# Optimization experiments

Measured on AMD Instinct MI355X. Metric: run time of the kernel, lower is better.

The kernel has to match this reference:

```python
import jax, jax.numpy as jnp
import numpy as np

B, T, N, D, TXT, TE, H = 8, 8192, 256, 512, 768, 2048, 8
DH = D // H


def _ln(x, g, b):
    m = jnp.mean(x, axis=-1, keepdims=True)
    v = jnp.mean(jnp.square(x - m), axis=-1, keepdims=True)
    return (x - m) * jax.lax.rsqrt(v + 1e-5) * g + b


def setup_inputs() -> dict:
    key = jax.random.key(0)
    ks = jax.random.split(key, 10)
    s = 0.02  # init scale for weights (zero_module init replaced by small random for a non-trivial baseline)
    return {
        "x": jax.random.normal(ks[0], (B, T, D), jnp.float32),
        "xf": jax.random.normal(ks[1], (B, N, TXT), jnp.float32),
        "emb": jax.random.normal(ks[2], (B, TE), jnp.float32),
        "ln_x_g": jnp.ones((D,), jnp.float32),
        "ln_x_b": jnp.zeros((D,), jnp.float32),
        "ln_t_g": jnp.ones((TXT,), jnp.float32),
        "ln_t_b": jnp.zeros((TXT,), jnp.float32),
        "Wq": jax.random.normal(ks[3], (D, D), jnp.float32) * s,
        "bq": jnp.zeros((D,), jnp.float32),
        "Wk": jax.random.normal(ks[4], (TXT, D), jnp.float32) * s,
        "bk": jnp.zeros((D,), jnp.float32),
        "Wv": jax.random.normal(ks[5], (TXT, D), jnp.float32) * s,
        "bv": jnp.zeros((D,), jnp.float32),
        "emb_W": jax.random.normal(ks[6], (TE, 2 * D), jnp.float32) * s,
        "emb_b": jnp.zeros((2 * D,), jnp.float32),
        "ln_o_g": jnp.ones((D,), jnp.float32),
        "ln_o_b": jnp.zeros((D,), jnp.float32),
        "out_W": jax.random.normal(ks[7], (D, D), jnp.float32) * s,
        "out_b": jnp.zeros((D,), jnp.float32),
    }


def reference(x, xf, emb, ln_x_g, ln_x_b, ln_t_g, ln_t_b, Wq, bq, Wk, bk, Wv, bv,
              emb_W, emb_b, ln_o_g, ln_o_b, out_W, out_b):
    xt = _ln(xf, ln_t_g, ln_t_b)                                  # [B,N,TXT]
    q = jax.nn.softmax((_ln(x, ln_x_g, ln_x_b) @ Wq + bq).reshape(B, T, H, DH), axis=-1)
    k = jax.nn.softmax((xt @ Wk + bk).reshape(B, N, H, DH), axis=-1)
    v = (xt @ Wv + bv).reshape(B, N, H, DH)
    attn = jnp.einsum('bnhd,bnhl->bhdl', k, v)                    # [B,H,DH,DH] kv aggregation
    out = jnp.einsum('bthd,bhdl->bthl', q, attn).reshape(B, T, D)  # [B,T,D]
    # StylizationBlock
    eo = (jax.nn.silu(emb) @ emb_W + emb_b)[:, None, :]           # [B,1,2D]
    scale, shift = jnp.split(eo, 2, axis=2)
    h = _ln(out, ln_o_g, ln_o_b) * (1 + scale) + shift
    h = jax.nn.silu(h) @ out_W + out_b
    return x + h
```

## Files before the change

kernel.cpp:

```cpp
#include <hip/hip_runtime.h>
#include <hip/hip_bf16.h>
#include <math.h>

#define Bc 8
#define Tc 8192
#define NTOK 256
#define Dc 512
#define TXT 768
#define TEc 2048
#define Hc 8
#define DHc 64
#define MROWS (Bc * Tc)

typedef __attribute__((ext_vector_type(8))) short bf16x8v;
typedef __attribute__((ext_vector_type(8))) unsigned short u16x8;
typedef __attribute__((ext_vector_type(4))) unsigned short u16x4;
typedef __attribute__((ext_vector_type(4))) float f32x4;

#define MFMA16(a, b, c) __builtin_amdgcn_mfma_f32_16x16x32_bf16(a, b, c, 0, 0, 0)

__device__ __forceinline__ unsigned short f2bf(float f) {
    __hip_bfloat16 h = __float2bfloat16(f);
    return __builtin_bit_cast(unsigned short, h);
}
__device__ __forceinline__ float bf2f(unsigned short u) {
    unsigned int x = ((unsigned int)u) << 16;
    return __builtin_bit_cast(float, x);
}

typedef __attribute__((address_space(3))) unsigned int lds_u32_t;
typedef __attribute__((address_space(1))) const unsigned int gbl_u32_t;
__device__ __forceinline__ void gload16(const unsigned short* g, short* l) {
    __builtin_amdgcn_global_load_lds((gbl_u32_t*)g, (lds_u32_t*)l, 16, 0, 0);
}

__device__ __forceinline__ float warp32_reduce_sum(float v) {
    v += __shfl_xor(v, 16); v += __shfl_xor(v, 8); v += __shfl_xor(v, 4);
    v += __shfl_xor(v, 2);  v += __shfl_xor(v, 1);
    return v;
}

__device__ __forceinline__ void transpose_tile(const float* __restrict__ src,
                                               unsigned short* __restrict__ dst,
                                               int N, int rs, int k0, int n0) {
    __shared__ float tile[64][65];
    int tx = threadIdx.x & 63, tq = threadIdx.x >> 6;
#pragma unroll
    for (int i = 0; i < 16; ++i) {
        int kk = tq + i * 4;
        tile[kk][tx] = src[(size_t)(k0 + kk) * N + n0 + tx];
    }
    __syncthreads();
#pragma unroll
    for (int i = 0; i < 16; ++i) {
        int nn = tq + i * 4;
        dst[(size_t)(n0 + nn) * rs + k0 + tx] = f2bf(tile[tx][nn]);
    }
}

__global__ void __launch_bounds__(256) prep_kernel(
    const float* __restrict__ Wq, const float* __restrict__ oW,
    const float* __restrict__ Wk, const float* __restrict__ Wv,
    const float* __restrict__ xf, const float* __restrict__ ln_t_g,
    const float* __restrict__ ln_t_b,
    unsigned short* __restrict__ Wqt, unsigned short* __restrict__ oWt,
    unsigned short* __restrict__ Wkvt, unsigned short* __restrict__ xt) {
    int bid = blockIdx.x;
    if (bid < 64) {
        transpose_tile(Wq, Wqt, Dc, Dc, (bid >> 3) * 64, (bid & 7) * 64);
        return;
    }
    if (bid < 128) {
        int i = bid - 64;
        transpose_tile(oW, oWt, Dc, Dc, (i >> 3) * 64, (i & 7) * 64);
        return;
    }
    if (bid < 224) {
        int i = bid - 128;
        transpose_tile(Wk, Wkvt, Dc, TXT, (i >> 3) * 64, (i & 7) * 64);
        return;
    }
    if (bid < 320) {
        int i = bid - 224;
        transpose_tile(Wv, Wkvt + (size_t)512 * TXT, Dc, TXT, (i >> 3) * 64, (i & 7) * 64);
        return;
    }
    int w = threadIdx.x >> 6, l = threadIdx.x & 63;
    int row = (bid - 320) * 4 + w;
    const float* src = xf + (size_t)row * TXT;
    float4 a0 = *(const float4*)&src[l * 12];
    float4 a1 = *(const float4*)&src[l * 12 + 4];
    float4 a2 = *(const float4*)&src[l * 12 + 8];
    float vals[12] = {a0.x, a0.y, a0.z, a0.w, a1.x, a1.y, a1.z, a1.w,
                      a2.x, a2.y, a2.z, a2.w};
    float s = 0.f, ss = 0.f;
#pragma unroll
    for (int j = 0; j < 12; ++j) { s += vals[j]; ss += vals[j] * vals[j]; }
#pragma unroll
    for (int m = 1; m <= 32; m <<= 1) { s += __shfl_xor(s, m); ss += __shfl_xor(ss, m); }
    float mean = s * (1.f / TXT), var = ss * (1.f / TXT) - mean * mean;
    float rs = rsqrtf(var + 1e-5f);
    unsigned short o[12];
#pragma unroll
    for (int j = 0; j < 12; ++j) {
        int c = l * 12 + j;
        o[j] = f2bf((vals[j] - mean) * rs * ln_t_g[c] + ln_t_b[c]);
    }
    unsigned short* dp = xt + (size_t)row * TXT + l * 12;
    *(u16x4*)&dp[0] = *(u16x4*)&o[0];
    *(u16x4*)&dp[4] = *(u16x4*)&o[4];
    *(u16x4*)&dp[8] = *(u16x4*)&o[8];
}

__global__ void __launch_bounds__(256) ln_x_kernel(const float* __restrict__ x,
                                                   const float* __restrict__ g,
                                                   const float* __restrict__ bt,
                                                   unsigned short* __restrict__ A1) {
    int w = threadIdx.x >> 6, l = threadIdx.x & 63;
    int row = blockIdx.x * 4 + w;
    const float* src = x + (size_t)row * Dc;
    float4 a0 = *(const float4*)&src[l * 8];
    float4 a1 = *(const float4*)&src[l * 8 + 4];
    float vals[8] = {a0.x, a0.y, a0.z, a0.w, a1.x, a1.y, a1.z, a1.w};
    float s = 0.f, ss = 0.f;
#pragma unroll
    for (int j = 0; j < 8; ++j) { s += vals[j]; ss += vals[j] * vals[j]; }
#pragma unroll
    for (int m = 1; m <= 32; m <<= 1) { s += __shfl_xor(s, m); ss += __shfl_xor(ss, m); }
    float mean = s * (1.f / Dc), var = ss * (1.f / Dc) - mean * mean;
    float rs = rsqrtf(var + 1e-5f);
    u16x8 o;
#pragma unroll
    for (int j = 0; j < 8; ++j) {
        int c = l * 8 + j;
        o[j] = f2bf((vals[j] - mean) * rs * g[c] + bt[c]);
    }
    *(u16x8*)&A1[(size_t)row * Dc + l * 8] = o;
}

__global__ void __launch_bounds__(256) kvgemm_kernel(
    const unsigned short* __restrict__ xt, const unsigned short* __restrict__ Wkvt,
    const float* __restrict__ bk, const float* __restrict__ bv,
    unsigned short* __restrict__ kbuf, unsigned short* __restrict__ vbuf) {
    __shared__ short lds_s[16384];
    short* Alds = lds_s;
    short* Blds = lds_s + 8192;

    const int tid = threadIdx.x, l = tid & 63, w = tid >> 6;
    const int lr = l & 15, lg = l >> 4;
    int mt = blockIdx.x >> 3, nt = blockIdx.x & 7;
    int row0 = mt * 128, col0 = nt * 128;
    int wrow = (w >> 1) * 64, wcol = (w & 1) * 64;

    f32x4 acc[4][4] = {};
    const int cbase = w * 64 + l;

    for (int ks = 0; ks < 12; ++ks) {
#pragma unroll
        for (int i = 0; i < 4; ++i) {
            int c = i * 256 + cbase;
            int r = c >> 3, kc = c & 7;
            int koff = ks * 64 + ((kc ^ (r & 7)) << 3);
            gload16(xt + (size_t)(row0 + r) * TXT + koff, &Alds[((i * 4 + w) * 64) * 8]);
            gload16(Wkvt + (size_t)(col0 + r) * TXT + koff, &Blds[((i * 4 + w) * 64) * 8]);
        }
        __syncthreads();
#pragma unroll
        for (int kk = 0; kk < 2; ++kk) {
            int kcw = kk * 4 + lg;
            bf16x8v af[4], bfr[4];
#pragma unroll
            for (int i = 0; i < 4; ++i) {
                int r = wrow + i * 16 + lr;
                af[i] = *(bf16x8v*)&Alds[(r * 8 + (kcw ^ (r & 7))) * 8];
            }
#pragma unroll
            for (int j = 0; j < 4; ++j) {
                int n = wcol + j * 16 + lr;
                bfr[j] = *(bf16x8v*)&Blds[(n * 8 + (kcw ^ (n & 7))) * 8];
            }
#pragma unroll
            for (int i = 0; i < 4; ++i)
#pragma unroll
                for (int j = 0; j < 4; ++j)
                    acc[i][j] = MFMA16(af[i], bfr[j], acc[i][j]);
        }
        __syncthreads();
    }

    const bool kHalf = (col0 + wcol) < 512;
    int cj[4];
    float bias[4];
#pragma unroll
    for (int j = 0; j < 4; ++j) {
        cj[j] = col0 + wcol + j * 16 + lr;
        bias[j] = kHalf ? bk[cj[j]] : bv[cj[j] - 512];
    }
#pragma unroll
    for (int i = 0; i < 4; ++i)
#pragma unroll
        for (int reg = 0; reg < 4; ++reg) {
            float v0 = acc[i][0][reg] + bias[0], v1 = acc[i][1][reg] + bias[1];
            float v2 = acc[i][2][reg] + bias[2], v3 = acc[i][3][reg] + bias[3];
            if (kHalf) {
                float m = fmaxf(fmaxf(v0, v1), fmaxf(v2, v3));
                m = fmaxf(m, __shfl_xor(m, 1)); m = fmaxf(m, __shfl_xor(m, 2));
                m = fmaxf(m, __shfl_xor(m, 4)); m = fmaxf(m, __shfl_xor(m, 8));
                float e0 = __expf(v0 - m), e1 = __expf(v1 - m);
                float e2 = __expf(v2 - m), e3 = __expf(v3 - m);
                float ssum = e0 + e1 + e2 + e3;
                ssum += __shfl_xor(ssum, 1); ssum += __shfl_xor(ssum, 2);
                ssum += __shfl_xor(ssum, 4); ssum += __shfl_xor(ssum, 8);
                float inv = 1.f / ssum;
                v0 = e0 * inv; v1 = e1 * inv; v2 = e2 * inv; v3 = e3 * inv;
            }
            int r = row0 + wrow + i * 16 + 4 * lg + reg;
            float vv[4] = {v0, v1, v2, v3};
#pragma unroll
            for (int j = 0; j < 4; ++j) {
                if (kHalf) kbuf[(size_t)r * Dc + cj[j]] = f2bf(vv[j]);
                else       vbuf[(size_t)r * Dc + cj[j] - 512] = f2bf(vv[j]);
            }
        }
}

__global__ void __launch_bounds__(512) attn_kernel(const unsigned short* __restrict__ kbuf,
                                                   const unsigned short* __restrict__ vbuf,
                                                   unsigned short* __restrict__ attn_t) {
    __shared__ unsigned short ksh[128][DHc], vsh[128][DHc];
    const int tid = threadIdx.x;
    const int b = blockIdx.x >> 3, h = blockIdx.x & 7;
    const int d = tid >> 3, lb = (tid & 7) * 8;
    const int tok = tid >> 2, c0 = (tid & 3) * 16;
    float acc[8] = {0.f};
    for (int st = 0; st < 2; ++st) {
        __syncthreads();
        size_t o = (size_t)(b * NTOK + st * 128 + tok) * Dc + h * DHc + c0;
        *(u16x8*)&ksh[tok][c0]     = *(const u16x8*)&kbuf[o];
        *(u16x8*)&ksh[tok][c0 + 8] = *(const u16x8*)&kbuf[o + 8];
        *(u16x8*)&vsh[tok][c0]     = *(const u16x8*)&vbuf[o];
        *(u16x8*)&vsh[tok][c0 + 8] = *(const u16x8*)&vbuf[o + 8];
        __syncthreads();
        for (int n = 0; n < 128; ++n) {
            float kd = bf2f(ksh[n][d]);
            u16x4 va = *(const u16x4*)&vsh[n][lb];
            u16x4 vb = *(const u16x4*)&vsh[n][lb + 4];
#pragma unroll
            for (int e = 0; e < 4; ++e) acc[e] += kd * bf2f(va[e]);
#pragma unroll
            for (int e = 0; e < 4; ++e) acc[4 + e] += kd * bf2f(vb[e]);
        }
    }
    size_t base = (size_t)(b * 8 + h) * DHc * DHc;
#pragma unroll
    for (int e = 0; e < 8; ++e)
        attn_t[base + (size_t)(lb + e) * DHc + d] = f2bf(acc[e]);
}

__global__ void __launch_bounds__(256) emb_kernel(const float* __restrict__ emb,
                                                  const float* __restrict__ emb_W,
                                                  const float* __restrict__ emb_b,
                                                  float* __restrict__ eo) {
    __shared__ float s[4][TEc];
    __shared__ float red[4][64][4];
    const int tid = threadIdx.x;
    const int chunk = blockIdx.x >> 1, bh = blockIdx.x & 1;
#pragma unroll
    for (int j = 0; j < 8; ++j) {
        int idx = tid + 256 * j;
        int bi = idx >> 9, kk4 = (idx & 511) * 4;
#pragma unroll
        for (int e = 0; e < 4; ++e) {
            float v = emb[(bh * 4 + bi) * TEc + kk4 + e];
            s[bi][kk4 + e] = v / (1.f + __expf(-v));
        }
    }
    __syncthreads();
    int c = tid & 63, q = tid >> 6;
    int col = chunk * 64 + c;
    float acc[4] = {0.f, 0.f, 0.f, 0.f};
    for (int kk = q * 512; kk < q * 512 + 512; ++kk) {
        float wv = emb_W[(size_t)kk * (2 * Dc) + col];
#pragma unroll
        for (int bi = 0; bi < 4; ++bi) acc[bi] += s[bi][kk] * wv;
    }
#pragma unroll
    for (int bi = 0; bi < 4; ++bi) red[q][c][bi] = acc[bi];
    __syncthreads();
    if (q == 0) {
        float bb = emb_b[col];
#pragma unroll
        for (int bi = 0; bi < 4; ++bi)
            eo[(bh * 4 + bi) * (2 * Dc) + col] =
                red[0][c][bi] + red[1][c][bi] + red[2][c][bi] + red[3][c][bi] + bb;
    }
}

__global__ void __launch_bounds__(512, 4) gemm1_kernel(
    const unsigned short* __restrict__ A1, const unsigned short* __restrict__ Wt,
    const float* __restrict__ bq, const unsigned short* __restrict__ attn_t,
    unsigned short* __restrict__ out1) {
    __shared__ short lds_s[24576];
    short* Alds = lds_s;
    short* Blds = lds_s + 16384;

    const int tid = threadIdx.x, l = tid & 63, w = tid >> 6;
    const int lr = l & 15, lg = l >> 4;
    int raw = blockIdx.x;
    int swz = (raw & 7) * 128 + (raw >> 3);
    int mt = swz >> 2, nt = swz & 3;
    int row0 = mt * 256, col0 = nt * 128;
    int b = row0 >> 13;
    int wrow = (w >> 1) * 64, wcol = (w & 1) * 64;

    f32x4 acc[4][4] = {};

    for (int ks = 0; ks < 8; ++ks) {
#pragma unroll
        for (int i = 0; i < 4; ++i) {
            int c = i * 512 + tid;
            int r = c >> 3, kc = c & 7;
            int koff = ks * 64 + ((kc ^ (r & 7)) << 3);
            gload16(A1 + (size_t)(row0 + r) * Dc + koff, &Alds[(i * 8 + w) * 512]);
        }
#pragma unroll
        for (int i = 0; i < 2; ++i) {
            int c = i * 512 + tid;
            int r = c >> 3, kc = c & 7;
            int koff = ks * 64 + ((kc ^ (r & 7)) << 3);
            gload16(Wt + (size_t)(col0 + r) * Dc + koff, &Blds[(i * 8 + w) * 512]);
        }
        __syncthreads();
#pragma unroll
        for (int kk = 0; kk < 2; ++kk) {
            int kcw = kk * 4 + lg;
            bf16x8v af[4], bfr[4];
#pragma unroll
            for (int i = 0; i < 4; ++i) {
                int r = wrow + i * 16 + lr;
                af[i] = *(bf16x8v*)&Alds[(r * 8 + (kcw ^ (r & 7))) * 8];
            }
#pragma unroll
            for (int j = 0; j < 4; ++j) {
                int n = wcol + j * 16 + lr;
                bfr[j] = *(bf16x8v*)&Blds[(n * 8 + (kcw ^ (n & 7))) * 8];
            }
#pragma unroll
            for (int i = 0; i < 4; ++i)
#pragma unroll
                for (int j = 0; j < 4; ++j)
                    acc[i][j] = MFMA16(af[i], bfr[j], acc[i][j]);
        }
        __syncthreads();
    }

    float bqv[4];
#pragma unroll
    for (int j = 0; j < 4; ++j) bqv[j] = bq[col0 + wcol + j * 16 + lr];

    int hw = nt * 2 + (w & 1);
    const unsigned short* at = attn_t + (size_t)(b * 8 + hw) * DHc * DHc;
    short* Qw = lds_s + w * 1024;

#pragma unroll
    for (int i = 0; i < 4; ++i) {
#pragma unroll
        for (int reg = 0; reg < 4; ++reg) {
            float v0 = acc[i][0][reg] + bqv[0], v1 = acc[i][1][reg] + bqv[1];
            float v2 = acc[i][2][reg] + bqv[2], v3 = acc[i][3][reg] + bqv[3];
            float m = fmaxf(fmaxf(v0, v1), fmaxf(v2, v3));
            m = fmaxf(m, __shfl_xor(m, 1)); m = fmaxf(m, __shfl_xor(m, 2));
            m = fmaxf(m, __shfl_xor(m, 4)); m = fmaxf(m, __shfl_xor(m, 8));
            float e0 = __expf(v0 - m), e1 = __expf(v1 - m);
            float e2 = __expf(v2 - m), e3 = __expf(v3 - m);
            float ssum = e0 + e1 + e2 + e3;
            ssum += __shfl_xor(ssum, 1); ssum += __shfl_xor(ssum, 2);
            ssum += __shfl_xor(ssum, 4); ssum += __shfl_xor(ssum, 8);
            float inv = 1.f / ssum;
            acc[i][0][reg] = e0 * inv; acc[i][1][reg] = e1 * inv;
            acc[i][2][reg] = e2 * inv; acc[i][3][reg] = e3 * inv;
        }
#pragma unroll
        for (int j = 0; j < 4; ++j)
#pragma unroll
            for (int reg = 0; reg < 4; ++reg) {
                int rl = 4 * lg + reg;
                int c = j * 16 + lr;
                Qw[(rl * 8 + ((c >> 3) ^ (rl & 7))) * 8 + (c & 7)] =
                    (short)f2bf(acc[i][j][reg]);
            }
        f32x4 acc2[4] = {};
#pragma unroll
        for (int kk = 0; kk < 2; ++kk) {
            int kc = kk * 4 + lg;
            bf16x8v a = *(bf16x8v*)&Qw[(lr * 8 + (kc ^ (lr & 7))) * 8];
            bf16x8v bf2[4];
#pragma unroll
            for (int j = 0; j < 4; ++j)
                bf2[j] = *(const bf16x8v*)&at[(j * 16 + lr) * DHc + kk * 32 + lg * 8];
#pragma unroll
            for (int j = 0; j < 4; ++j)
                acc2[j] = MFMA16(a, bf2[j], acc2[j]);
        }
#pragma unroll
        for (int j = 0; j < 4; ++j)
#pragma unroll
            for (int reg = 0; reg < 4; ++reg) {
                int r = row0 + wrow + i * 16 + 4 * lg + reg;
                int c = col0 + wcol + j * 16 + lr;
                out1[(size_t)r * Dc + c] = f2bf(acc2[j][reg]);
            }
    }
}

__global__ void __launch_bounds__(256) mid_kernel(const unsigned short* __restrict__ out1,
                                                  const float* __restrict__ eo,
                                                  const float* __restrict__ g,
                                                  const float* __restrict__ bt,
                                                  unsigned short* __restrict__ A2) {
    int w = threadIdx.x >> 6, l = threadIdx.x & 63;
    int row = blockIdx.x * 4 + w;
    int b = row >> 13;
    u16x8 iv = *(const u16x8*)&out1[(size_t)row * Dc + l * 8];
    float vals[8];
    float s = 0.f, ss = 0.f;
#pragma unroll
    for (int j = 0; j < 8; ++j) {
        vals[j] = bf2f(iv[j]);
        s += vals[j]; ss += vals[j] * vals[j];
    }
#pragma unroll
    for (int m = 1; m <= 32; m <<= 1) { s += __shfl_xor(s, m); ss += __shfl_xor(ss, m); }
    float mean = s * (1.f / Dc), var = ss * (1.f / Dc) - mean * mean;
    float rs = rsqrtf(var + 1e-5f);
    const float* scl = eo + (size_t)b * (2 * Dc);
    const float* shf = scl + Dc;
    u16x8 o;
#pragma unroll
    for (int j = 0; j < 8; ++j) {
        int c = l * 8 + j;
        float t = (vals[j] - mean) * rs * g[c] + bt[c];
        t = t * (1.f + scl[c]) + shf[c];
        t = t / (1.f + __expf(-t));
        o[j] = f2bf(t);
    }
    *(u16x8*)&A2[(size_t)row * Dc + l * 8] = o;
}

__global__ void __launch_bounds__(512, 4) gemm2_kernel(
    const unsigned short* __restrict__ A2, const unsigned short* __restrict__ Wt,
    const float* __restrict__ ob, const float* __restrict__ x,
    float* __restrict__ out) {
    __shared__ short lds_s[24576];
    short* Alds = lds_s;
    short* Blds = lds_s + 16384;

    const int tid = threadIdx.x, l = tid & 63, w = tid >> 6;
    const int lr = l & 15, lg = l >> 4;
    int raw = blockIdx.x;
    int swz = (raw & 7) * 128 + (raw >> 3);
    int mt = swz >> 2, nt = swz & 3;
    int row0 = mt * 256, col0 = nt * 128;
    int wrow = (w >> 1) * 64, wcol = (w & 1) * 64;

    f32x4 acc[4][4] = {};

    for (int ks = 0; ks < 8; ++ks) {
#pragma unroll
        for (int i = 0; i < 4; ++i) {
            int c = i * 512 + tid;
            int r = c >> 3, kc = c & 7;
            int koff = ks * 64 + ((kc ^ (r & 7)) << 3);
            gload16(A2 + (size_t)(row0 + r) * Dc + koff, &Alds[(i * 8 + w) * 512]);
        }
#pragma unroll
        for (int i = 0; i < 2; ++i) {
            int c = i * 512 + tid;
            int r = c >> 3, kc = c & 7;
            int koff = ks * 64 + ((kc ^ (r & 7)) << 3);
            gload16(Wt + (size_t)(col0 + r) * Dc + koff, &Blds[(i * 8 + w) * 512]);
        }
        __syncthreads();
#pragma unroll
        for (int kk = 0; kk < 2; ++kk) {
            int kcw = kk * 4 + lg;
            bf16x8v af[4], bfr[4];
#pragma unroll
            for (int i = 0; i < 4; ++i) {
                int r = wrow + i * 16 + lr;
                af[i] = *(bf16x8v*)&Alds[(r * 8 + (kcw ^ (r & 7))) * 8];
            }
#pragma unroll
            for (int j = 0; j < 4; ++j) {
                int n = wcol + j * 16 + lr;
                bfr[j] = *(bf16x8v*)&Blds[(n * 8 + (kcw ^ (n & 7))) * 8];
            }
#pragma unroll
            for (int i = 0; i < 4; ++i)
#pragma unroll
                for (int j = 0; j < 4; ++j)
                    acc[i][j] = MFMA16(af[i], bfr[j], acc[i][j]);
        }
        __syncthreads();
    }

    float obv[4];
#pragma unroll
    for (int j = 0; j < 4; ++j) obv[j] = ob[col0 + wcol + j * 16 + lr];
#pragma unroll
    for (int i = 0; i < 4; ++i)
#pragma unroll
        for (int j = 0; j < 4; ++j)
#pragma unroll
            for (int reg = 0; reg < 4; ++reg) {
                int r = row0 + wrow + i * 16 + 4 * lg + reg;
                int c = col0 + wcol + j * 16 + lr;
                size_t o = (size_t)r * Dc + c;
                out[o] = acc[i][j][reg] + obv[j] + x[o];
            }
}

extern "C" void kernel_launch(void* const* d_in, const int* in_sizes, int n_in,
                              void* d_out, int out_size, void* d_ws, size_t ws_size,
                              hipStream_t stream) {
    const float* x      = (const float*)d_in[0];
    const float* xf     = (const float*)d_in[1];
    const float* emb    = (const float*)d_in[2];
    const float* ln_x_g = (const float*)d_in[3];
    const float* ln_x_b = (const float*)d_in[4];
    const float* ln_t_g = (const float*)d_in[5];
    const float* ln_t_b = (const float*)d_in[6];
    const float* Wq     = (const float*)d_in[7];
    const float* bq     = (const float*)d_in[8];
    const float* Wk     = (const float*)d_in[9];
    const float* bk     = (const float*)d_in[10];
    const float* Wv     = (const float*)d_in[11];
    const float* bv     = (const float*)d_in[12];
    const float* emb_W  = (const float*)d_in[13];
    const float* emb_b  = (const float*)d_in[14];
    const float* ln_o_g = (const float*)d_in[15];
    const float* ln_o_b = (const float*)d_in[16];
    const float* out_W  = (const float*)d_in[17];
    const float* out_b  = (const float*)d_in[18];
    float* out = (float*)d_out;

    unsigned short* xt   = (unsigned short*)d_ws;
    unsigned short* kbuf = xt + (size_t)2048 * TXT;
    unsigned short* vbuf = kbuf + (size_t)2048 * 512;
    unsigned short* Wkvt = vbuf + (size_t)2048 * 512;
    unsigned short* Wqt  = Wkvt + (size_t)1024 * TXT;
    unsigned short* oWt  = Wqt + (size_t)512 * 512;
    unsigned short* attn_t = oWt + (size_t)512 * 512;
    float* eo = (float*)(attn_t + (size_t)64 * 64 * 64);
    unsigned short* out1 = (unsigned short*)(eo + 8 * 1024);
    unsigned short* A1   = out1 + (size_t)MROWS * Dc;
    unsigned short* A2   = A1;

    hipLaunchKernelGGL(prep_kernel, dim3(832), dim3(256), 0, stream,
                       Wq, out_W, Wk, Wv, xf, ln_t_g, ln_t_b, Wqt, oWt, Wkvt, xt);
    hipLaunchKernelGGL(ln_x_kernel, dim3(MROWS / 4), dim3(256), 0, stream,
                       x, ln_x_g, ln_x_b, A1);
    hipLaunchKernelGGL(kvgemm_kernel, dim3(16 * 8), dim3(256), 0, stream,
                       xt, Wkvt, bk, bv, kbuf, vbuf);
    hipLaunchKernelGGL(attn_kernel, dim3(Bc * Hc), dim3(512), 0, stream,
                       kbuf, vbuf, attn_t);
    hipLaunchKernelGGL(emb_kernel, dim3(32), dim3(256), 0, stream, emb, emb_W, emb_b, eo);
    hipLaunchKernelGGL(gemm1_kernel, dim3(MROWS / 256 * 4), dim3(512), 0, stream,
                       A1, Wqt, bq, attn_t, out1);
    hipLaunchKernelGGL(mid_kernel, dim3(MROWS / 4), dim3(256), 0, stream,
                       out1, eo, ln_o_g, ln_o_b, A2);
    hipLaunchKernelGGL(gemm2_kernel, dim3(MROWS / 256 * 4), dim3(512), 0, stream,
                       A2, oWt, out_b, x, out);
}
```

Baseline: 298.5 us.

## Double-buffer LDS tiles and shrink GEMM blocks to 128x128 with 256 threads

Both large GEMM kernels now prefetch the next K-slice into a second LDS buffer with async global-to-LDS loads while MFMAs run on the current slice. This replaces the old load-then-sync-then-compute loop. Block tiles drop from 256x128 with 512 threads to 128x128 with 256 threads, launch bounds change, and the grid doubles. The aim is to hide global load latency behind compute and improve scheduling, at the cost of more LDS per block and more redundant weight-tile loads.

```diff
diff --git a/kernel.cpp b/kernel.cpp
--- a/kernel.cpp
+++ b/kernel.cpp
@@ -32,12 +32,6 @@
 typedef __attribute__((address_space(1))) const unsigned int gbl_u32_t;
 __device__ __forceinline__ void gload16(const unsigned short* g, short* l) {
     __builtin_amdgcn_global_load_lds((gbl_u32_t*)g, (lds_u32_t*)l, 16, 0, 0);
-}
-
-__device__ __forceinline__ float warp32_reduce_sum(float v) {
-    v += __shfl_xor(v, 16); v += __shfl_xor(v, 8); v += __shfl_xor(v, 4);
-    v += __shfl_xor(v, 2);  v += __shfl_xor(v, 1);
-    return v;
 }
 
 __device__ __forceinline__ void transpose_tile(const float* __restrict__ src,
@@ -296,41 +290,56 @@
     }
 }
 
-__global__ void __launch_bounds__(512, 4) gemm1_kernel(
+
+__global__ void __launch_bounds__(256, 2) gemm1_kernel(
     const unsigned short* __restrict__ A1, const unsigned short* __restrict__ Wt,
     const float* __restrict__ bq, const unsigned short* __restrict__ attn_t,
     unsigned short* __restrict__ out1) {
-    __shared__ short lds_s[24576];
-    short* Alds = lds_s;
-    short* Blds = lds_s + 16384;
+    __shared__ short lds_s[32768];
 
     const int tid = threadIdx.x, l = tid & 63, w = tid >> 6;
     const int lr = l & 15, lg = l >> 4;
     int raw = blockIdx.x;
-    int swz = (raw & 7) * 128 + (raw >> 3);
+    int swz = (raw & 7) * 256 + (raw >> 3);
     int mt = swz >> 2, nt = swz & 3;
-    int row0 = mt * 256, col0 = nt * 128;
+    int row0 = mt * 128, col0 = nt * 128;
     int b = row0 >> 13;
     int wrow = (w >> 1) * 64, wcol = (w & 1) * 64;
+    const int cbase = w * 64 + l;
 
     f32x4 acc[4][4] = {};
 
+    {
+        short* Ad = lds_s;
+        short* Bd = lds_s + 8192;
+#pragma unroll
+        for (int i = 0; i < 4; ++i) {
+            int c = i * 256 + cbase;
+            int r = c >> 3, kc = c & 7;
+            int koff = ((kc ^ (r & 7)) << 3);
+            gload16(A1 + (size_t)(row0 + r) * Dc + koff, &Ad[((i * 4 + w) * 64) * 8]);
+            gload16(Wt + (size_t)(col0 + r) * Dc + koff, &Bd[((i * 4 + w) * 64) * 8]);
+        }
+    }
+    __syncthreads();
+
     for (int ks = 0; ks < 8; ++ks) {
-#pragma unroll
-        for (int i = 0; i < 4; ++i) {
-            int c = i * 512 + tid;
-            int r = c >> 3, kc = c & 7;
-            int koff = ks * 64 + ((kc ^ (r & 7)) << 3);
-            gload16(A1 + (size_t)(row0 + r) * Dc + koff, &Alds[(i * 8 + w) * 512]);
-        }
-#pragma unroll
-        for (int i = 0; i < 2; ++i) {
-            int c = i * 512 + tid;
-            int r = c >> 3, kc = c & 7;
-            int koff = ks * 64 + ((kc ^ (r & 7)) << 3);
-            gload16(Wt + (size_t)(col0 + r) * Dc + koff, &Blds[(i * 8 + w) * 512]);
-        }
-        __syncthreads();
+        int cur = ks & 1;
+        if (ks < 7) {
+            short* Ad = lds_s + (cur ^ 1) * 16384;
+            short* Bd = Ad + 8192;
+            int koff0 = (ks + 1) * 64;
+#pragma unroll
+            for (int i = 0; i < 4; ++i) {
+                int c = i * 256 + cbase;
+                int r = c >> 3, kc = c & 7;
+                int koff = koff0 + ((kc ^ (r & 7)) << 3);
+                gload16(A1 + (size_t)(row0 + r) * Dc + koff, &Ad[((i * 4 + w) * 64) * 8]);
+                gload16(Wt + (size_t)(col0 + r) * Dc + koff, &Bd[((i * 4 + w) * 64) * 8]);
+            }
+        }
+        short* Alds = lds_s + cur * 16384;
+        short* Blds = Alds + 8192;
 #pragma unroll
         for (int kk = 0; kk < 2; ++kk) {
             int kcw = kk * 4 + lg;
@@ -358,7 +367,7 @@
 #pragma unroll
     for (int j = 0; j < 4; ++j) bqv[j] = bq[col0 + wcol + j * 16 + lr];
 
-    int hw = nt * 2 + (w & 1);
+    int hw = nt * 2 + (wcol >> 6);
     const unsigned short* at = attn_t + (size_t)(b * 8 + hw) * DHc * DHc;
     short* Qw = lds_s + w * 1024;
 
@@ -447,40 +456,54 @@
     *(u16x8*)&A2[(size_t)row * Dc + l * 8] = o;
 }
 
-__global__ void __launch_bounds__(512, 4) gemm2_kernel(
+__global__ void __launch_bounds__(256, 2) gemm2_kernel(
     const unsigned short* __restrict__ A2, const unsigned short* __restrict__ Wt,
     const float* __restrict__ ob, const float* __restrict__ x,
     float* __restrict__ out) {
-    __shared__ short lds_s[24576];
-    short* Alds = lds_s;
-    short* Blds = lds_s + 16384;
+    __shared__ short lds_s[32768];
 
     const int tid = threadIdx.x, l = tid & 63, w = tid >> 6;
     const int lr = l & 15, lg = l >> 4;
     int raw = blockIdx.x;
-    int swz = (raw & 7) * 128 + (raw >> 3);
+    int swz = (raw & 7) * 256 + (raw >> 3);
     int mt = swz >> 2, nt = swz & 3;
-    int row0 = mt * 256, col0 = nt * 128;
+    int row0 = mt * 128, col0 = nt * 128;
     int wrow = (w >> 1) * 64, wcol = (w & 1) * 64;
+    const int cbase = w * 64 + l;
 
     f32x4 acc[4][4] = {};
 
+    {
+        short* Ad = lds_s;
+        short* Bd = lds_s + 8192;
+#pragma unroll
+        for (int i = 0; i < 4; ++i) {
+            int c = i * 256 + cbase;
+            int r = c >> 3, kc = c & 7;
+            int koff = ((kc ^ (r & 7)) << 3);
+            gload16(A2 + (size_t)(row0 + r) * Dc + koff, &Ad[((i * 4 + w) * 64) * 8]);
+            gload16(Wt + (size_t)(col0 + r) * Dc + koff, &Bd[((i * 4 + w) * 64) * 8]);
+        }
+    }
+    __syncthreads();
+
     for (int ks = 0; ks < 8; ++ks) {
-#pragma unroll
-        for (int i = 0; i < 4; ++i) {
-            int c = i * 512 + tid;
-            int r = c >> 3, kc = c & 7;
-            int koff = ks * 64 + ((kc ^ (r & 7)) << 3);
-            gload16(A2 + (size_t)(row0 + r) * Dc + koff, &Alds[(i * 8 + w) * 512]);
-        }
-#pragma unroll
-        for (int i = 0; i < 2; ++i) {
-            int c = i * 512 + tid;
-            int r = c >> 3, kc = c & 7;
-            int koff = ks * 64 + ((kc ^ (r & 7)) << 3);
-            gload16(Wt + (size_t)(col0 + r) * Dc + koff, &Blds[(i * 8 + w) * 512]);
-        }
-        __syncthreads();
+        int cur = ks & 1;
+        if (ks < 7) {
+            short* Ad = lds_s + (cur ^ 1) * 16384;
+            short* Bd = Ad + 8192;
+            int koff0 = (ks + 1) * 64;
+#pragma unroll
+            for (int i = 0; i < 4; ++i) {
+                int c = i * 256 + cbase;
+                int r = c >> 3, kc = c & 7;
+                int koff = koff0 + ((kc ^ (r & 7)) << 3);
+                gload16(A2 + (size_t)(row0 + r) * Dc + koff, &Ad[((i * 4 + w) * 64) * 8]);
+                gload16(Wt + (size_t)(col0 + r) * Dc + koff, &Bd[((i * 4 + w) * 64) * 8]);
+            }
+        }
+        short* Alds = lds_s + cur * 16384;
+        short* Blds = Alds + 8192;
 #pragma unroll
         for (int kk = 0; kk < 2; ++kk) {
             int kcw = kk * 4 + lg;
@@ -565,10 +588,10 @@
     hipLaunchKernelGGL(attn_kernel, dim3(Bc * Hc), dim3(512), 0, stream,
                        kbuf, vbuf, attn_t);
     hipLaunchKernelGGL(emb_kernel, dim3(32), dim3(256), 0, stream, emb, emb_W, emb_b, eo);
-    hipLaunchKernelGGL(gemm1_kernel, dim3(MROWS / 256 * 4), dim3(512), 0, stream,
+    hipLaunchKernelGGL(gemm1_kernel, dim3(MROWS / 128 * 4), dim3(256), 0, stream,
                        A1, Wqt, bq, attn_t, out1);
     hipLaunchKernelGGL(mid_kernel, dim3(MROWS / 4), dim3(256), 0, stream,
                        out1, eo, ln_o_g, ln_o_b, A2);
-    hipLaunchKernelGGL(gemm2_kernel, dim3(MROWS / 256 * 4), dim3(512), 0, stream,
+    hipLaunchKernelGGL(gemm2_kernel, dim3(MROWS / 128 * 4), dim3(256), 0, stream,
                        A2, oWt, out_b, x, out);
 }
```

Result: slower. 307.8 us (median of 4 runs) (+3.1%).

## Fuse input LayerNorm, Q GEMM/attention and output LN+modulation into one kernel

Applied to the files above, without the earlier changes.

The separate ln_x and mid kernels are removed. The Q GEMM kernel now computes the input LayerNorm from fp32 x in registers and stores it into LDS. It uses 64-row tiles that span the full 512 output columns, so the output LayerNorm statistics can be reduced inside the block, and it applies the scale/shift and SiLU before writing A2. This removes the write and read of the A1 and out1 intermediates and saves two launches. In exchange it loads the full Wq matrix per 64-row block, cuts A reuse per block, and uses more LDS, which may lower occupancy.

```diff
diff --git a/kernel.cpp b/kernel.cpp
--- a/kernel.cpp
+++ b/kernel.cpp
@@ -32,12 +32,6 @@
 typedef __attribute__((address_space(1))) const unsigned int gbl_u32_t;
 __device__ __forceinline__ void gload16(const unsigned short* g, short* l) {
     __builtin_amdgcn_global_load_lds((gbl_u32_t*)g, (lds_u32_t*)l, 16, 0, 0);
-}
-
-__device__ __forceinline__ float warp32_reduce_sum(float v) {
-    v += __shfl_xor(v, 16); v += __shfl_xor(v, 8); v += __shfl_xor(v, 4);
-    v += __shfl_xor(v, 2);  v += __shfl_xor(v, 1);
-    return v;
 }
 
 __device__ __forceinline__ void transpose_tile(const float* __restrict__ src,
@@ -110,32 +104,6 @@
     *(u16x4*)&dp[0] = *(u16x4*)&o[0];
     *(u16x4*)&dp[4] = *(u16x4*)&o[4];
     *(u16x4*)&dp[8] = *(u16x4*)&o[8];
-}
-
-__global__ void __launch_bounds__(256) ln_x_kernel(const float* __restrict__ x,
-                                                   const float* __restrict__ g,
-                                                   const float* __restrict__ bt,
-                                                   unsigned short* __restrict__ A1) {
-    int w = threadIdx.x >> 6, l = threadIdx.x & 63;
-    int row = blockIdx.x * 4 + w;
-    const float* src = x + (size_t)row * Dc;
-    float4 a0 = *(const float4*)&src[l * 8];
-    float4 a1 = *(const float4*)&src[l * 8 + 4];
-    float vals[8] = {a0.x, a0.y, a0.z, a0.w, a1.x, a1.y, a1.z, a1.w};
-    float s = 0.f, ss = 0.f;
-#pragma unroll
-    for (int j = 0; j < 8; ++j) { s += vals[j]; ss += vals[j] * vals[j]; }
-#pragma unroll
-    for (int m = 1; m <= 32; m <<= 1) { s += __shfl_xor(s, m); ss += __shfl_xor(ss, m); }
-    float mean = s * (1.f / Dc), var = ss * (1.f / Dc) - mean * mean;
-    float rs = rsqrtf(var + 1e-5f);
-    u16x8 o;
-#pragma unroll
-    for (int j = 0; j < 8; ++j) {
-        int c = l * 8 + j;
-        o[j] = f2bf((vals[j] - mean) * rs * g[c] + bt[c]);
-    }
-    *(u16x8*)&A1[(size_t)row * Dc + l * 8] = o;
 }
 
 __global__ void __launch_bounds__(256) kvgemm_kernel(
@@ -296,39 +264,64 @@
     }
 }
 
-__global__ void __launch_bounds__(512, 4) gemm1_kernel(
-    const unsigned short* __restrict__ A1, const unsigned short* __restrict__ Wt,
+__global__ void __launch_bounds__(512, 4) gemm1m_kernel(
+    const float* __restrict__ x, const float* __restrict__ lng,
+    const float* __restrict__ lnb, const unsigned short* __restrict__ Wt,
     const float* __restrict__ bq, const unsigned short* __restrict__ attn_t,
-    unsigned short* __restrict__ out1) {
-    __shared__ short lds_s[24576];
+    const float* __restrict__ eo, const float* __restrict__ go_,
+    const float* __restrict__ bo_, unsigned short* __restrict__ A2) {
+    __shared__ short lds_s[36864];
     short* Alds = lds_s;
-    short* Blds = lds_s + 16384;
+    short* Blds = lds_s + 4096;
 
     const int tid = threadIdx.x, l = tid & 63, w = tid >> 6;
     const int lr = l & 15, lg = l >> 4;
-    int raw = blockIdx.x;
-    int swz = (raw & 7) * 128 + (raw >> 3);
-    int mt = swz >> 2, nt = swz & 3;
-    int row0 = mt * 256, col0 = nt * 128;
-    int b = row0 >> 13;
-    int wrow = (w >> 1) * 64, wcol = (w & 1) * 64;
+    const int row0 = blockIdx.x * 64;
+    const int b = row0 >> 13;
+    const int wcol = w * 64;
+
+    bf16x8v xr[8];
+    {
+        float4 g0 = *(const float4*)&lng[l * 8], g1 = *(const float4*)&lng[l * 8 + 4];
+        float4 b0 = *(const float4*)&lnb[l * 8], b1 = *(const float4*)&lnb[l * 8 + 4];
+        float gg[8] = {g0.x, g0.y, g0.z, g0.w, g1.x, g1.y, g1.z, g1.w};
+        float bb[8] = {b0.x, b0.y, b0.z, b0.w, b1.x, b1.y, b1.z, b1.w};
+#pragma unroll
+        for (int rr = 0; rr < 8; ++rr) {
+            const float* src = x + (size_t)(row0 + w * 8 + rr) * Dc + l * 8;
+            float4 a0 = *(const float4*)&src[0];
+            float4 a1 = *(const float4*)&src[4];
+            float vals[8] = {a0.x, a0.y, a0.z, a0.w, a1.x, a1.y, a1.z, a1.w};
+            float s = 0.f, ss = 0.f;
+#pragma unroll
+            for (int j = 0; j < 8; ++j) { s += vals[j]; ss += vals[j] * vals[j]; }
+#pragma unroll
+            for (int m = 1; m <= 32; m <<= 1) { s += __shfl_xor(s, m); ss += __shfl_xor(ss, m); }
+            float mean = s * (1.f / Dc), var = ss * (1.f / Dc) - mean * mean;
+            float rsq = rsqrtf(var + 1e-5f);
+#pragma unroll
+            for (int j = 0; j < 8; ++j)
+                xr[rr][j] = (short)f2bf((vals[j] - mean) * rsq * gg[j] + bb[j]);
+        }
+    }
 
     f32x4 acc[4][4] = {};
 
     for (int ks = 0; ks < 8; ++ks) {
-#pragma unroll
-        for (int i = 0; i < 4; ++i) {
+        if ((l >> 3) == ks) {
+            int kc = l & 7;
+#pragma unroll
+            for (int rr = 0; rr < 8; ++rr) {
+                int r = w * 8 + rr;
+                *(bf16x8v*)&Alds[(r * 8 + (kc ^ (r & 7))) * 8] = xr[rr];
+            }
+        }
+#pragma unroll
+        for (int i = 0; i < 8; ++i) {
             int c = i * 512 + tid;
             int r = c >> 3, kc = c & 7;
             int koff = ks * 64 + ((kc ^ (r & 7)) << 3);
-            gload16(A1 + (size_t)(row0 + r) * Dc + koff, &Alds[(i * 8 + w) * 512]);
-        }
-#pragma unroll
-        for (int i = 0; i < 2; ++i) {
-            int c = i * 512 + tid;
-            int r = c >> 3, kc = c & 7;
-            int koff = ks * 64 + ((kc ^ (r & 7)) << 3);
-            gload16(Wt + (size_t)(col0 + r) * Dc + koff, &Blds[(i * 8 + w) * 512]);
+            gload16(Wt + (size_t)r * Dc + koff, &Blds[((i * 8 + w) * 64) * 8]);
         }
         __syncthreads();
 #pragma unroll
@@ -337,7 +330,7 @@
             bf16x8v af[4], bfr[4];
 #pragma unroll
             for (int i = 0; i < 4; ++i) {
-                int r = wrow + i * 16 + lr;
+                int r = i * 16 + lr;
                 af[i] = *(bf16x8v*)&Alds[(r * 8 + (kcw ^ (r & 7))) * 8];
             }
 #pragma unroll
@@ -356,11 +349,9 @@
 
     float bqv[4];
 #pragma unroll
-    for (int j = 0; j < 4; ++j) bqv[j] = bq[col0 + wcol + j * 16 + lr];
-
-    int hw = nt * 2 + (w & 1);
-    const unsigned short* at = attn_t + (size_t)(b * 8 + hw) * DHc * DHc;
-    short* Qw = lds_s + w * 1024;
+    for (int j = 0; j < 4; ++j) bqv[j] = bq[wcol + j * 16 + lr];
+    const unsigned short* at = attn_t + (size_t)(b * 8 + w) * DHc * DHc;
+    short* Qw = Blds + w * 1024;
 
 #pragma unroll
     for (int i = 0; i < 4; ++i) {
@@ -403,48 +394,59 @@
                 acc2[j] = MFMA16(a, bf2[j], acc2[j]);
         }
 #pragma unroll
-        for (int j = 0; j < 4; ++j)
-#pragma unroll
-            for (int reg = 0; reg < 4; ++reg) {
-                int r = row0 + wrow + i * 16 + 4 * lg + reg;
-                int c = col0 + wcol + j * 16 + lr;
-                out1[(size_t)r * Dc + c] = f2bf(acc2[j][reg]);
-            }
-    }
-}
-
-__global__ void __launch_bounds__(256) mid_kernel(const unsigned short* __restrict__ out1,
-                                                  const float* __restrict__ eo,
-                                                  const float* __restrict__ g,
-                                                  const float* __restrict__ bt,
-                                                  unsigned short* __restrict__ A2) {
-    int w = threadIdx.x >> 6, l = threadIdx.x & 63;
-    int row = blockIdx.x * 4 + w;
-    int b = row >> 13;
-    u16x8 iv = *(const u16x8*)&out1[(size_t)row * Dc + l * 8];
-    float vals[8];
-    float s = 0.f, ss = 0.f;
-#pragma unroll
-    for (int j = 0; j < 8; ++j) {
-        vals[j] = bf2f(iv[j]);
-        s += vals[j]; ss += vals[j] * vals[j];
-    }
-#pragma unroll
-    for (int m = 1; m <= 32; m <<= 1) { s += __shfl_xor(s, m); ss += __shfl_xor(ss, m); }
-    float mean = s * (1.f / Dc), var = ss * (1.f / Dc) - mean * mean;
-    float rs = rsqrtf(var + 1e-5f);
+        for (int j = 0; j < 4; ++j) acc[i][j] = acc2[j];
+    }
+
+    float* pstat = (float*)Alds;
+#pragma unroll
+    for (int i = 0; i < 4; ++i)
+#pragma unroll
+        for (int reg = 0; reg < 4; ++reg) {
+            float s = acc[i][0][reg] + acc[i][1][reg] + acc[i][2][reg] + acc[i][3][reg];
+            float ss = acc[i][0][reg] * acc[i][0][reg] + acc[i][1][reg] * acc[i][1][reg]
+                     + acc[i][2][reg] * acc[i][2][reg] + acc[i][3][reg] * acc[i][3][reg];
+            s += __shfl_xor(s, 1); ss += __shfl_xor(ss, 1);
+            s += __shfl_xor(s, 2); ss += __shfl_xor(ss, 2);
+            s += __shfl_xor(s, 4); ss += __shfl_xor(ss, 4);
+            s += __shfl_xor(s, 8); ss += __shfl_xor(ss, 8);
+            if (lr == 0) {
+                int rloc = i * 16 + 4 * lg + reg;
+                pstat[(rloc * 8 + w) * 2 + 0] = s;
+                pstat[(rloc * 8 + w) * 2 + 1] = ss;
+            }
+        }
+    __syncthreads();
+
     const float* scl = eo + (size_t)b * (2 * Dc);
     const float* shf = scl + Dc;
-    u16x8 o;
-#pragma unroll
-    for (int j = 0; j < 8; ++j) {
-        int c = l * 8 + j;
-        float t = (vals[j] - mean) * rs * g[c] + bt[c];
-        t = t * (1.f + scl[c]) + shf[c];
-        t = t / (1.f + __expf(-t));
-        o[j] = f2bf(t);
-    }
-    *(u16x8*)&A2[(size_t)row * Dc + l * 8] = o;
+    float go[4], bo[4], sc[4], sh[4];
+#pragma unroll
+    for (int j = 0; j < 4; ++j) {
+        int c = wcol + j * 16 + lr;
+        go[j] = go_[c]; bo[j] = bo_[c]; sc[j] = scl[c]; sh[j] = shf[c];
+    }
+#pragma unroll
+    for (int i = 0; i < 4; ++i)
+#pragma unroll
+        for (int reg = 0; reg < 4; ++reg) {
+            int rloc = i * 16 + 4 * lg + reg;
+            float s = 0.f, ss = 0.f;
+#pragma unroll
+            for (int q = 0; q < 8; ++q) {
+                s += pstat[(rloc * 8 + q) * 2 + 0];
+                ss += pstat[(rloc * 8 + q) * 2 + 1];
+            }
+            float mean = s * (1.f / Dc), var = ss * (1.f / Dc) - mean * mean;
+            float rsq = rsqrtf(var + 1e-5f);
+            size_t rowoff = (size_t)(row0 + rloc) * Dc;
+#pragma unroll
+            for (int j = 0; j < 4; ++j) {
+                float t = (acc[i][j][reg] - mean) * rsq * go[j] + bo[j];
+                t = t * (1.f + sc[j]) + sh[j];
+                t = t / (1.f + __expf(-t));
+                A2[rowoff + wcol + j * 16 + lr] = f2bf(t);
+            }
+        }
 }
 
 __global__ void __launch_bounds__(512, 4) gemm2_kernel(
@@ -552,23 +554,17 @@
     unsigned short* oWt  = Wqt + (size_t)512 * 512;
     unsigned short* attn_t = oWt + (size_t)512 * 512;
     float* eo = (float*)(attn_t + (size_t)64 * 64 * 64);
-    unsigned short* out1 = (unsigned short*)(eo + 8 * 1024);
-    unsigned short* A1   = out1 + (size_t)MROWS * Dc;
-    unsigned short* A2   = A1;
+    unsigned short* A2 = (unsigned short*)(eo + 8 * 1024);
 
     hipLaunchKernelGGL(prep_kernel, dim3(832), dim3(256), 0, stream,
                        Wq, out_W, Wk, Wv, xf, ln_t_g, ln_t_b, Wqt, oWt, Wkvt, xt);
-    hipLaunchKernelGGL(ln_x_kernel, dim3(MROWS / 4), dim3(256), 0, stream,
-                       x, ln_x_g, ln_x_b, A1);
     hipLaunchKernelGGL(kvgemm_kernel, dim3(16 * 8), dim3(256), 0, stream,
                        xt, Wkvt, bk, bv, kbuf, vbuf);
     hipLaunchKernelGGL(attn_kernel, dim3(Bc * Hc), dim3(512), 0, stream,
                        kbuf, vbuf, attn_t);
     hipLaunchKernelGGL(emb_kernel, dim3(32), dim3(256), 0, stream, emb, emb_W, emb_b, eo);
-    hipLaunchKernelGGL(gemm1_kernel, dim3(MROWS / 256 * 4), dim3(512), 0, stream,
-                       A1, Wqt, bq, attn_t, out1);
-    hipLaunchKernelGGL(mid_kernel, dim3(MROWS / 4), dim3(256), 0, stream,
-                       out1, eo, ln_o_g, ln_o_b, A2);
+    hipLaunchKernelGGL(gemm1m_kernel, dim3(MROWS / 64), dim3(512), 0, stream,
+                       x, ln_x_g, ln_x_b, Wqt, bq, attn_t, eo, ln_o_g, ln_o_b, A2);
     hipLaunchKernelGGL(gemm2_kernel, dim3(MROWS / 256 * 4), dim3(512), 0, stream,
                        A2, oWt, out_b, x, out);
 }
```

Measured after the change: 310.7 us. +4.1%, slower.

## Merge ln_x and emb kernels into prep kernel and prefetch residual x in gemm2

Applied to the files above, without the earlier changes.

Folds the x LayerNorm and the embedding projection into the prep kernel as extra block ranges sharing one shared-memory buffer, removing two launches and letting the small emb work overlap the large LN work. In gemm2 it adds volatile loads of the residual x tile during later K-steps to warm the cache before the epilogue reads it. The prep kernel's shared-memory footprint grows to 36KB for all blocks, which may lower occupancy for the LN blocks. The prefetch adds extra global traffic per K-step. A gemm1 head index is also rewritten equivalently.

```diff
diff --git a/kernel.cpp b/kernel.cpp
--- a/kernel.cpp
+++ b/kernel.cpp
@@ -34,16 +34,11 @@
     __builtin_amdgcn_global_load_lds((gbl_u32_t*)g, (lds_u32_t*)l, 16, 0, 0);
 }
 
-__device__ __forceinline__ float warp32_reduce_sum(float v) {
-    v += __shfl_xor(v, 16); v += __shfl_xor(v, 8); v += __shfl_xor(v, 4);
-    v += __shfl_xor(v, 2);  v += __shfl_xor(v, 1);
-    return v;
-}
-
 __device__ __forceinline__ void transpose_tile(const float* __restrict__ src,
                                                unsigned short* __restrict__ dst,
-                                               int N, int rs, int k0, int n0) {
-    __shared__ float tile[64][65];
+                                               int N, int rs, int k0, int n0,
+                                               char* smem) {
+    float (*tile)[65] = (float(*)[65])smem;
     int tx = threadIdx.x & 63, tq = threadIdx.x >> 6;
 #pragma unroll
     for (int i = 0; i < 16; ++i) {
@@ -55,6 +50,46 @@
     for (int i = 0; i < 16; ++i) {
         int nn = tq + i * 4;
         dst[(size_t)(n0 + nn) * rs + k0 + tx] = f2bf(tile[tx][nn]);
+    }
+}
+
+__device__ __forceinline__ void emb_block(int bid, const float* __restrict__ emb,
+                                          const float* __restrict__ emb_W,
+                                          const float* __restrict__ emb_b,
+                                          float* __restrict__ eo, char* smem) {
+    float* s   = (float*)smem;
+    float* red = (float*)(smem + 32768);
+    const int tid = threadIdx.x;
+    const int chunk = bid >> 1, bh = bid & 1;
+#pragma unroll
+    for (int j = 0; j < 8; ++j) {
+        int idx = tid + 256 * j;
+        int bi = idx >> 9, kk4 = (idx & 511) * 4;
+#pragma unroll
+        for (int e = 0; e < 4; ++e) {
+            float v = emb[(bh * 4 + bi) * TEc + kk4 + e];
+            s[bi * TEc + kk4 + e] = v / (1.f + __expf(-v));
+        }
+    }
+    __syncthreads();
+    int c = tid & 63, q = tid >> 6;
+    int col = chunk * 64 + c;
+    float acc[4] = {0.f, 0.f, 0.f, 0.f};
+    for (int kk = q * 512; kk < q * 512 + 512; ++kk) {
+        float wv = emb_W[(size_t)kk * (2 * Dc) + col];
+#pragma unroll
+        for (int bi = 0; bi < 4; ++bi) acc[bi] += s[bi * TEc + kk] * wv;
+    }
+#pragma unroll
+    for (int bi = 0; bi < 4; ++bi) red[(q * 64 + c) * 4 + bi] = acc[bi];
+    __syncthreads();
+    if (q == 0) {
+        float bb = emb_b[col];
+#pragma unroll
+        for (int bi = 0; bi < 4; ++bi)
+            eo[(bh * 4 + bi) * (2 * Dc) + col] =
+                red[(0 * 64 + c) * 4 + bi] + red[(1 * 64 + c) * 4 + bi] +
+                red[(2 * 64 + c) * 4 + bi] + red[(3 * 64 + c) * 4 + bi] + bb;
     }
 }
 
@@ -64,78 +99,86 @@
     const float* __restrict__ xf, const float* __restrict__ ln_t_g,
     const float* __restrict__ ln_t_b,
     unsigned short* __restrict__ Wqt, unsigned short* __restrict__ oWt,
-    unsigned short* __restrict__ Wkvt, unsigned short* __restrict__ xt) {
+    unsigned short* __restrict__ Wkvt, unsigned short* __restrict__ xt,
+    const float* __restrict__ emb, const float* __restrict__ emb_W,
+    const float* __restrict__ emb_b, float* __restrict__ eo,
+    const float* __restrict__ x, const float* __restrict__ ln_x_g,
+    const float* __restrict__ ln_x_b, unsigned short* __restrict__ A1) {
+    __shared__ __align__(16) char smem[36864];
     int bid = blockIdx.x;
     if (bid < 64) {
-        transpose_tile(Wq, Wqt, Dc, Dc, (bid >> 3) * 64, (bid & 7) * 64);
+        transpose_tile(Wq, Wqt, Dc, Dc, (bid >> 3) * 64, (bid & 7) * 64, smem);
         return;
     }
     if (bid < 128) {
         int i = bid - 64;
-        transpose_tile(oW, oWt, Dc, Dc, (i >> 3) * 64, (i & 7) * 64);
+        transpose_tile(oW, oWt, Dc, Dc, (i >> 3) * 64, (i & 7) * 64, smem);
         return;
     }
     if (bid < 224) {
         int i = bid - 128;
-        transpose_tile(Wk, Wkvt, Dc, TXT, (i >> 3) * 64, (i & 7) * 64);
+        transpose_tile(Wk, Wkvt, Dc, TXT, (i >> 3) * 64, (i & 7) * 64, smem);
         return;
     }
     if (bid < 320) {
         int i = bid - 224;
-        transpose_tile(Wv, Wkvt + (size_t)512 * TXT, Dc, TXT, (i >> 3) * 64, (i & 7) * 64);
+        transpose_tile(Wv, Wkvt + (size_t)512 * TXT, Dc, TXT, (i >> 3) * 64, (i & 7) * 64, smem);
         return;
     }
-    int w = threadIdx.x >> 6, l = threadIdx.x & 63;
-    int row = (bid - 320) * 4 + w;
-    const float* src = xf + (size_t)row * TXT;
-    float4 a0 = *(const float4*)&src[l * 12];
-    float4 a1 = *(const float4*)&src[l * 12 + 4];
-    float4 a2 = *(const float4*)&src[l * 12 + 8];
-    float vals[12] = {a0.x, a0.y, a0.z, a0.w, a1.x, a1.y, a1.z, a1.w,
-                      a2.x, a2.y, a2.z, a2.w};
-    float s = 0.f, ss = 0.f;
-#pragma unroll
-    for (int j = 0; j < 12; ++j) { s += vals[j]; ss += vals[j] * vals[j]; }
-#pragma unroll
-    for (int m = 1; m <= 32; m <<= 1) { s += __shfl_xor(s, m); ss += __shfl_xor(ss, m); }
-    float mean = s * (1.f / TXT), var = ss * (1.f / TXT) - mean * mean;
-    float rs = rsqrtf(var + 1e-5f);
-    unsigned short o[12];
-#pragma unroll
-    for (int j = 0; j < 12; ++j) {
-        int c = l * 12 + j;
-        o[j] = f2bf((vals[j] - mean) * rs * ln_t_g[c] + ln_t_b[c]);
-    }
-    unsigned short* dp = xt + (size_t)row * TXT + l * 12;
-    *(u16x4*)&dp[0] = *(u16x4*)&o[0];
-    *(u16x4*)&dp[4] = *(u16x4*)&o[4];
-    *(u16x4*)&dp[8] = *(u16x4*)&o[8];
-}
-
-__global__ void __launch_bounds__(256) ln_x_kernel(const float* __restrict__ x,
-                                                   const float* __restrict__ g,
-                                                   const float* __restrict__ bt,
-                                                   unsigned short* __restrict__ A1) {
-    int w = threadIdx.x >> 6, l = threadIdx.x & 63;
-    int row = blockIdx.x * 4 + w;
-    const float* src = x + (size_t)row * Dc;
-    float4 a0 = *(const float4*)&src[l * 8];
-    float4 a1 = *(const float4*)&src[l * 8 + 4];
-    float vals[8] = {a0.x, a0.y, a0.z, a0.w, a1.x, a1.y, a1.z, a1.w};
-    float s = 0.f, ss = 0.f;
-#pragma unroll
-    for (int j = 0; j < 8; ++j) { s += vals[j]; ss += vals[j] * vals[j]; }
-#pragma unroll
-    for (int m = 1; m <= 32; m <<= 1) { s += __shfl_xor(s, m); ss += __shfl_xor(ss, m); }
-    float mean = s * (1.f / Dc), var = ss * (1.f / Dc) - mean * mean;
-    float rs = rsqrtf(var + 1e-5f);
-    u16x8 o;
-#pragma unroll
-    for (int j = 0; j < 8; ++j) {
-        int c = l * 8 + j;
-        o[j] = f2bf((vals[j] - mean) * rs * g[c] + bt[c]);
-    }
-    *(u16x8*)&A1[(size_t)row * Dc + l * 8] = o;
+    if (bid < 832) {
+        int w = threadIdx.x >> 6, l = threadIdx.x & 63;
+        int row = (bid - 320) * 4 + w;
+        const float* src = xf + (size_t)row * TXT;
+        float4 a0 = *(const float4*)&src[l * 12];
+        float4 a1 = *(const float4*)&src[l * 12 + 4];
+        float4 a2 = *(const float4*)&src[l * 12 + 8];
+        float vals[12] = {a0.x, a0.y, a0.z, a0.w, a1.x, a1.y, a1.z, a1.w,
+                          a2.x, a2.y, a2.z, a2.w};
+        float s = 0.f, ss = 0.f;
+#pragma unroll
+        for (int j = 0; j < 12; ++j) { s += vals[j]; ss += vals[j] * vals[j]; }
+#pragma unroll
+        for (int m = 1; m <= 32; m <<= 1) { s += __shfl_xor(s, m); ss += __shfl_xor(ss, m); }
+        float mean = s * (1.f / TXT), var = ss * (1.f / TXT) - mean * mean;
+        float rs = rsqrtf(var + 1e-5f);
+        unsigned short o[12];
+#pragma unroll
+        for (int j = 0; j < 12; ++j) {
+            int c = l * 12 + j;
+            o[j] = f2bf((vals[j] - mean) * rs * ln_t_g[c] + ln_t_b[c]);
+        }
+        unsigned short* dp = xt + (size_t)row * TXT + l * 12;
+        *(u16x4*)&dp[0] = *(u16x4*)&o[0];
+        *(u16x4*)&dp[4] = *(u16x4*)&o[4];
+        *(u16x4*)&dp[8] = *(u16x4*)&o[8];
+        return;
+    }
+    if (bid < 864) {
+        emb_block(bid - 832, emb, emb_W, emb_b, eo, smem);
+        return;
+    }
+    {
+        int w = threadIdx.x >> 6, l = threadIdx.x & 63;
+        int row = (bid - 864) * 4 + w;
+        const float* src = x + (size_t)row * Dc;
+        float4 a0 = *(const float4*)&src[l * 8];
+        float4 a1 = *(const float4*)&src[l * 8 + 4];
+        float vals[8] = {a0.x, a0.y, a0.z, a0.w, a1.x, a1.y, a1.z, a1.w};
+        float s = 0.f, ss = 0.f;
+#pragma unroll
+        for (int j = 0; j < 8; ++j) { s += vals[j]; ss += vals[j] * vals[j]; }
+#pragma unroll
+        for (int m = 1; m <= 32; m <<= 1) { s += __shfl_xor(s, m); ss += __shfl_xor(ss, m); }
+        float mean = s * (1.f / Dc), var = ss * (1.f / Dc) - mean * mean;
+        float rs = rsqrtf(var + 1e-5f);
+        u16x8 o;
+#pragma unroll
+        for (int j = 0; j < 8; ++j) {
+            int c = l * 8 + j;
+            o[j] = f2bf((vals[j] - mean) * rs * ln_x_g[c] + ln_x_b[c]);
+        }
+        *(u16x8*)&A1[(size_t)row * Dc + l * 8] = o;
+    }
 }
 
 __global__ void __launch_bounds__(256) kvgemm_kernel(
@@ -257,45 +300,6 @@
         attn_t[base + (size_t)(lb + e) * DHc + d] = f2bf(acc[e]);
 }
 
-__global__ void __launch_bounds__(256) emb_kernel(const float* __restrict__ emb,
-                                                  const float* __restrict__ emb_W,
-                                                  const float* __restrict__ emb_b,
-                                                  float* __restrict__ eo) {
-    __shared__ float s[4][TEc];
-    __shared__ float red[4][64][4];
-    const int tid = threadIdx.x;
-    const int chunk = blockIdx.x >> 1, bh = blockIdx.x & 1;
-#pragma unroll
-    for (int j = 0; j < 8; ++j) {
-        int idx = tid + 256 * j;
-        int bi = idx >> 9, kk4 = (idx & 511) * 4;
-#pragma unroll
-        for (int e = 0; e < 4; ++e) {
-            float v = emb[(bh * 4 + bi) * TEc + kk4 + e];
-            s[bi][kk4 + e] = v / (1.f + __expf(-v));
-        }
-    }
-    __syncthreads();
-    int c = tid & 63, q = tid >> 6;
-    int col = chunk * 64 + c;
-    float acc[4] = {0.f, 0.f, 0.f, 0.f};
-    for (int kk = q * 512; kk < q * 512 + 512; ++kk) {
-        float wv = emb_W[(size_t)kk * (2 * Dc) + col];
-#pragma unroll
-        for (int bi = 0; bi < 4; ++bi) acc[bi] += s[bi][kk] * wv;
-    }
-#pragma unroll
-    for (int bi = 0; bi < 4; ++bi) red[q][c][bi] = acc[bi];
-    __syncthreads();
-    if (q == 0) {
-        float bb = emb_b[col];
-#pragma unroll
-        for (int bi = 0; bi < 4; ++bi)
-            eo[(bh * 4 + bi) * (2 * Dc) + col] =
-                red[0][c][bi] + red[1][c][bi] + red[2][c][bi] + red[3][c][bi] + bb;
-    }
-}
-
 __global__ void __launch_bounds__(512, 4) gemm1_kernel(
     const unsigned short* __restrict__ A1, const unsigned short* __restrict__ Wt,
     const float* __restrict__ bq, const unsigned short* __restrict__ attn_t,
@@ -358,7 +362,7 @@
 #pragma unroll
     for (int j = 0; j < 4; ++j) bqv[j] = bq[col0 + wcol + j * 16 + lr];
 
-    int hw = nt * 2 + (w & 1);
+    int hw = nt * 2 + (wcol >> 6);
     const unsigned short* at = attn_t + (size_t)(b * 8 + hw) * DHc * DHc;
     short* Qw = lds_s + w * 1024;
 
@@ -464,6 +468,7 @@
     int wrow = (w >> 1) * 64, wcol = (w & 1) * 64;
 
     f32x4 acc[4][4] = {};
+    const volatile float* xv = x;
 
     for (int ks = 0; ks < 8; ++ks) {
 #pragma unroll
@@ -479,6 +484,17 @@
             int r = c >> 3, kc = c & 7;
             int koff = ks * 64 + ((kc ^ (r & 7)) << 3);
             gload16(Wt + (size_t)(col0 + r) * Dc + koff, &Blds[(i * 8 + w) * 512]);
+        }
+        if (ks >= 4) {
+            int i = ks - 4;
+            size_t xbase = (size_t)(row0 + wrow + i * 16 + 4 * lg) * Dc + col0 + wcol + lr;
+#pragma unroll
+            for (int reg = 0; reg < 4; ++reg)
+#pragma unroll
+                for (int j = 0; j < 4; ++j) {
+                    float t = xv[xbase + (size_t)reg * Dc + j * 16];
+                    asm volatile("" :: "v"(t));
+                }
         }
         __syncthreads();
 #pragma unroll
@@ -556,15 +572,13 @@
     unsigned short* A1   = out1 + (size_t)MROWS * Dc;
     unsigned short* A2   = A1;
 
-    hipLaunchKernelGGL(prep_kernel, dim3(832), dim3(256), 0, stream,
-                       Wq, out_W, Wk, Wv, xf, ln_t_g, ln_t_b, Wqt, oWt, Wkvt, xt);
-    hipLaunchKernelGGL(ln_x_kernel, dim3(MROWS / 4), dim3(256), 0, stream,
-                       x, ln_x_g, ln_x_b, A1);
+    hipLaunchKernelGGL(prep_kernel, dim3(864 + MROWS / 4), dim3(256), 0, stream,
+                       Wq, out_W, Wk, Wv, xf, ln_t_g, ln_t_b, Wqt, oWt, Wkvt, xt,
+                       emb, emb_W, emb_b, eo, x, ln_x_g, ln_x_b, A1);
     hipLaunchKernelGGL(kvgemm_kernel, dim3(16 * 8), dim3(256), 0, stream,
                        xt, Wkvt, bk, bv, kbuf, vbuf);
     hipLaunchKernelGGL(attn_kernel, dim3(Bc * Hc), dim3(512), 0, stream,
                        kbuf, vbuf, attn_t);
-    hipLaunchKernelGGL(emb_kernel, dim3(32), dim3(256), 0, stream, emb, emb_W, emb_b, eo);
     hipLaunchKernelGGL(gemm1_kernel, dim3(MROWS / 256 * 4), dim3(512), 0, stream,
                        A1, Wqt, bq, attn_t, out1);
     hipLaunchKernelGGL(mid_kernel, dim3(MROWS / 4), dim3(256), 0, stream,
```

Result: slower. 498.7 us (+67.1%).
